# Kernel tuning notes

Hardware: AMD Instinct MI355X
Metric: run time of the kernel (lower is better)

The kernel has to match this reference:

```python
import jax, jax.numpy as jnp
import numpy as np

N = 200000      # total points
B = 4           # number of point clouds
C_IN = 128
C_OUT = 256
GRID = 0.05
EPS = 1e-5      # BatchNorm eps


def setup_inputs() -> dict:
    key = jax.random.key(0)
    ks = jax.random.split(key, 9)
    xyz = jax.random.uniform(ks[0], (1, N, 3), dtype=jnp.float32)
    features = jax.random.normal(ks[1], (1, N, C_IN), dtype=jnp.float32)
    offset = jnp.array([50000, 100000, 150000, 200000], dtype=jnp.int32)
    W1 = jax.random.normal(ks[2], (C_OUT, C_IN), dtype=jnp.float32) * 0.02
    b1 = jax.random.normal(ks[3], (C_OUT,), dtype=jnp.float32) * 0.01
    gamma = jax.random.uniform(ks[4], (C_OUT,), dtype=jnp.float32, minval=0.5, maxval=1.5)
    beta = jax.random.normal(ks[5], (C_OUT,), dtype=jnp.float32) * 0.1
    W2 = jax.random.normal(ks[6], (C_OUT, C_OUT), dtype=jnp.float32) * 0.02
    b2 = jax.random.normal(ks[7], (C_OUT,), dtype=jnp.float32) * 0.01
    return {"xyz": xyz, "features": features, "offset": offset,
            "W1": W1, "b1": b1, "gamma": gamma, "beta": beta, "W2": W2, "b2": b2}


def _offset2batch(offset, n):
    counts = jnp.diff(jnp.concatenate([jnp.zeros((1,), offset.dtype), offset]))
    return jnp.repeat(jnp.arange(offset.shape[0], dtype=jnp.int32), counts,
                      total_repeat_length=n)


def reference(xyz, features, offset, W1, b1, gamma, beta, W2, b2):
    pos = xyz[0]          # [N, 3]
    x = features[0]       # [N, C_IN]
    batch = _offset2batch(offset, pos.shape[0])  # [N]

    # fc: 1x1 conv == linear; BatchNorm1d in training mode (batch stats, biased var)
    h = x @ W1.T + b1                                   # [N, C_OUT]
    mu = h.mean(axis=0)
    var = h.var(axis=0)
    h = (h - mu) / jnp.sqrt(var + EPS) * gamma + beta
    h = jax.nn.relu(h)
    feats = h @ W2.T + b2                               # [N, C_OUT]

    # per-batch min corner (start)
    start = jax.ops.segment_min(pos, batch, num_segments=B)   # [B, 3]

    # voxel grid clustering
    coords = jnp.floor((pos - start[batch]) / GRID).astype(jnp.int32)  # [N, 3] >= 0
    dims = coords.max(axis=0) + 1
    lin = ((batch * dims[0] + coords[:, 0]) * dims[1] + coords[:, 1]) * dims[2] + coords[:, 2]

    uniq, inv, counts = jnp.unique(lin, return_inverse=True, return_counts=True)
    M = uniq.shape[0]

    # segment_csr mean / max over voxels (order-independent, equals sorted CSR reduce)
    xyz_out = jax.ops.segment_sum(pos, inv, num_segments=M) / counts[:, None].astype(pos.dtype)
    feat_out = jax.ops.segment_max(feats, inv, num_segments=M)

    seg_batch = jax.ops.segment_max(batch, inv, num_segments=M)
    offset_out = jnp.cumsum(jnp.bincount(seg_batch, length=B)).astype(offset.dtype)

    return (xyz_out[None], feat_out[None], offset_out, inv)
```

## Files before the change

### kernel.cpp

```cpp
#include <hip/hip_runtime.h>
#include <stdint.h>

#define GRID_SZ 0.05f
#define BN_EPS 1e-5f
#define FLAG_MAGIC 0x7FECA110

typedef __attribute__((ext_vector_type(8))) short bf16x8;
typedef __attribute__((ext_vector_type(4))) float f32x4;

#define WS_START   0
#define WS_DIMS    64
#define WS_CHSUM   128
#define WS_CHSQ    1152
#define WS_AC      2176
#define WS_BC      3200
#define WS_W1B     4224
#define WS_W2B     69760
#define WS_GRAM    200832
#define WS_CSUM    266368
#define WS_HIST    266880
#define WS_RANK    529024
#define WS_CURS    791296
#define WS_BSUM    1053440
#define WS_XYZS    1053952
#define WS_LIN     1840384
#define WS_PERM    2640384
#define WS_XB      3440384

__device__ __forceinline__ short f2bf(float f) {
  unsigned u = __float_as_uint(f);
  u += 0x7FFFu + ((u >> 16) & 1u);
  return (short)(u >> 16);
}

__device__ __forceinline__ bf16x8 load_frag(const float* p) {
  f32x4 a = *(const f32x4*)p;
  f32x4 b = *(const f32x4*)(p + 4);
  bf16x8 r;
  r[0] = f2bf(a[0]); r[1] = f2bf(a[1]); r[2] = f2bf(a[2]); r[3] = f2bf(a[3]);
  r[4] = f2bf(b[0]); r[5] = f2bf(b[1]); r[6] = f2bf(b[2]); r[7] = f2bf(b[3]);
  return r;
}

__device__ __forceinline__ int batch_of(int p, const int* offs, int nb) {
  int b = 0;
  while (b < nb - 1 && p >= offs[b]) b++;
  return b;
}

__device__ __forceinline__ float dec16(unsigned e) {
  unsigned us = (e & 0x8000u) ? (e & 0x7FFFu) : (~e & 0xFFFFu);
  return __uint_as_float(us << 16);
}

__global__ void k_conv(const float* __restrict__ src, short* __restrict__ dst, size_t n8) {
  size_t i = (size_t)blockIdx.x * blockDim.x + threadIdx.x;
  size_t stride = (size_t)gridDim.x * blockDim.x;
  for (; i < n8; i += stride)
    *(bf16x8*)(dst + i * 8) = load_frag(src + i * 8);
}

__global__ void k_convw(const float* __restrict__ W1, const float* __restrict__ W2,
                        short* __restrict__ W1b, short* __restrict__ W2b) {
  int i = blockIdx.x * blockDim.x + threadIdx.x;
  if (i < 4096) *(bf16x8*)(W1b + i * 8) = load_frag(W1 + i * 8);
  else { int j = i - 4096; *(bf16x8*)(W2b + j * 8) = load_frag(W2 + j * 8); }
}

__global__ void k_init(unsigned* featU, size_t featN, int* hist, float* xyzs,
                       float* chsum, float* chsq, float* gram, float* csum,
                       unsigned* gstart, int* gdims) {
  size_t i = (size_t)blockIdx.x * blockDim.x + threadIdx.x;
  size_t stride = (size_t)gridDim.x * blockDim.x;
  for (size_t j = i; j < featN; j += stride) featU[j] = 0u;
  for (size_t j = i; j < 65536; j += stride) hist[j] = 0;
  for (size_t j = i; j < 65536u * 3; j += stride) xyzs[j] = 0.f;
  for (size_t j = i; j < 16384; j += stride) gram[j] = 0.f;
  if (i < 256) { chsum[i] = 0.f; chsq[i] = 0.f; }
  if (i < 128) csum[i] = 0.f;
  if (i < 12) gstart[i] = 0x7F800000u;
  if (i < 3) gdims[i] = 0;
}

__global__ void k_min(const float* __restrict__ pos, const int* __restrict__ offs,
                      int N, int nb, unsigned* gstart) {
  __shared__ unsigned smin[12];
  int tid = threadIdx.x;
  if (tid < 12) smin[tid] = 0x7F800000u;
  __syncthreads();
  int p = blockIdx.x * blockDim.x + tid;
  if (p < N) {
    int b = batch_of(p, offs, nb);
    for (int c = 0; c < 3; c++)
      atomicMin(&smin[b * 3 + c], __float_as_uint(pos[p * 3 + c]));
  }
  __syncthreads();
  if (tid < 3 * nb) atomicMin(&gstart[tid], smin[tid]);
}

__global__ void k_dims(const float* __restrict__ pos, const int* __restrict__ offs,
                       int N, int nb, const unsigned* gstart, int* gdims) {
  __shared__ int sd[3];
  int tid = threadIdx.x;
  if (tid < 3) sd[tid] = 0;
  __syncthreads();
  int p = blockIdx.x * blockDim.x + tid;
  if (p < N) {
    int b = batch_of(p, offs, nb);
    for (int c = 0; c < 3; c++) {
      float s = __uint_as_float(gstart[b * 3 + c]);
      int cc = (int)floorf((pos[p * 3 + c] - s) / GRID_SZ);
      atomicMax(&sd[c], cc);
    }
  }
  __syncthreads();
  if (tid < 3) atomicMax(&gdims[tid], sd[tid]);
}

__global__ void k_hist(const float* __restrict__ pos, const int* __restrict__ offs,
                       int N, int nb, const unsigned* gstart, const int* gdims,
                       int* lin, int* hist, float* xyzs) {
  int p = blockIdx.x * blockDim.x + threadIdx.x;
  if (p >= N) return;
  int b = batch_of(p, offs, nb);
  int d0 = gdims[0] + 1, d1 = gdims[1] + 1, d2 = gdims[2] + 1;
  int c[3];
  for (int i = 0; i < 3; i++) {
    float s = __uint_as_float(gstart[b * 3 + i]);
    c[i] = (int)floorf((pos[p * 3 + i] - s) / GRID_SZ);
  }
  int li = ((b * d0 + c[0]) * d1 + c[1]) * d2 + c[2];
  if (li < 0 || li >= 65536) li = 0;
  lin[p] = li;
  atomicAdd(&hist[li], 1);
  atomicAdd(&xyzs[li * 3 + 0], pos[p * 3 + 0]);
  atomicAdd(&xyzs[li * 3 + 1], pos[p * 3 + 1]);
  atomicAdd(&xyzs[li * 3 + 2], pos[p * 3 + 2]);
}

__global__ __launch_bounds__(1024) void k_scanA(const int* __restrict__ hist,
                                                const int* __restrict__ gdims, int nb,
                                                int2* bsum) {
  __shared__ int so[16], sc2[16];
  int d0 = gdims[0] + 1, d1 = gdims[1] + 1, d2 = gdims[2] + 1;
  int bins = nb * d0 * d1 * d2;
  if (bins > 65536) bins = 65536;
  int i = blockIdx.x * 1024 + threadIdx.x;
  int o = 0, c = 0;
  if (i < bins) { int h = hist[i]; o = (h > 0); c = h; }
  for (int d = 1; d < 64; d <<= 1) { o += __shfl_xor(o, d); c += __shfl_xor(c, d); }
  int w = threadIdx.x >> 6;
  if ((threadIdx.x & 63) == 0) { so[w] = o; sc2[w] = c; }
  __syncthreads();
  if (threadIdx.x == 0) {
    int O = 0, C = 0;
    for (int k = 0; k < 16; k++) { O += so[k]; C += sc2[k]; }
    bsum[blockIdx.x] = make_int2(O, C);
  }
}

__global__ __launch_bounds__(1024) void k_scanB(const int* __restrict__ hist,
                                                const int* __restrict__ gdims, int nb,
                                                const int2* __restrict__ bsum,
                                                int* rank, int* cursor) {
  __shared__ int so[1024], sc2[1024];
  __shared__ int sbase[2];
  int d0 = gdims[0] + 1, d1 = gdims[1] + 1, d2 = gdims[2] + 1;
  int bins = nb * d0 * d1 * d2;
  if (bins > 65536) bins = 65536;
  int b = blockIdx.x;
  int tid = threadIdx.x;
  if (tid == 0) {
    int O = 0, C = 0;
    for (int k = 0; k < b; k++) { int2 s = bsum[k]; O += s.x; C += s.y; }
    sbase[0] = O; sbase[1] = C;
  }
  int i = b * 1024 + tid;
  int h = (i < bins) ? hist[i] : 0;
  int o = (h > 0), c = h;
  so[tid] = o; sc2[tid] = c;
  __syncthreads();
  for (int off = 1; off < 1024; off <<= 1) {
    int vo = (tid >= off) ? so[tid - off] : 0;
    int vc = (tid >= off) ? sc2[tid - off] : 0;
    __syncthreads();
    so[tid] += vo; sc2[tid] += vc;
    __syncthreads();
  }
  if (i < bins) {
    rank[i]   = sbase[0] + so[tid] - o;
    cursor[i] = sbase[1] + sc2[tid] - c;
  }
  if (i == bins - 1) rank[bins] = sbase[0] + so[tid];
}

__global__ void k_scatter(const int* __restrict__ lin, const int* __restrict__ rank,
                          int* cursor, int N, int* __restrict__ perm,
                          float* __restrict__ out_inv) {
  int p = blockIdx.x * blockDim.x + threadIdx.x;
  if (p >= N) return;
  int li = lin[p];
  out_inv[p] = (float)rank[li];
  int slot = atomicAdd(&cursor[li], 1);
  perm[slot] = p;
}

__global__ void k_voxfin(const int* __restrict__ hist, const int* __restrict__ rank,
                         const float* __restrict__ xyzs, const int* __restrict__ gdims,
                         int nb, float* out_xyz, float* out_off) {
  int d0 = gdims[0] + 1, d1 = gdims[1] + 1, d2 = gdims[2] + 1;
  int dxyz = d0 * d1 * d2;
  int bins = nb * dxyz;
  if (bins > 65536) bins = 65536;
  int i = blockIdx.x * blockDim.x + threadIdx.x;
  if (blockIdx.x == 0 && (int)threadIdx.x < nb) {
    int t = (int)threadIdx.x;
    int idx = (t + 1) * dxyz; if (idx > bins) idx = bins;
    out_off[t] = (float)rank[idx];
  }
  if (i >= bins) return;
  int cnt = hist[i];
  if (cnt <= 0) return;
  int v = rank[i];
  float fc = (float)cnt;
  out_xyz[v * 3 + 0] = xyzs[i * 3 + 0] / fc;
  out_xyz[v * 3 + 1] = xyzs[i * 3 + 1] / fc;
  out_xyz[v * 3 + 2] = xyzs[i * 3 + 2] / fc;
}

#define GCHUNK 1024
__global__ __launch_bounds__(256, 2) void k_gram(const short* __restrict__ Xb, int N,
                                                 float* __restrict__ gram,
                                                 float* __restrict__ csum) {
  __shared__ short xt[128 * 72];
  __shared__ float lcs[128];
  int tid = threadIdx.x;
  int wid = tid >> 6, lane = tid & 63;
  int lr = lane & 15, lg = lane >> 4;
  int base = blockIdx.x * GCHUNK;
  int cg = tid & 7;
  float cs[16];
#pragma unroll
  for (int j = 0; j < 16; j++) cs[j] = 0.f;
  f32x4 acc[2][8];
#pragma unroll
  for (int a = 0; a < 2; a++)
#pragma unroll
    for (int b = 0; b < 8; b++) acc[a][b] = (f32x4){0.f, 0.f, 0.f, 0.f};

  for (int k0 = 0; k0 < GCHUNK; k0 += 64) {
    __syncthreads();
#pragma unroll
    for (int it = 0; it < 2; it++) {
      int task = tid + it * 256;
      int r = task >> 3;
      int row = base + k0 + r;
      bf16x8 v0 = {0,0,0,0,0,0,0,0}, v1 = {0,0,0,0,0,0,0,0};
      if (row < N) {
        const short* src = Xb + (size_t)row * 128 + cg * 16;
        v0 = *(const bf16x8*)src;
        v1 = *(const bf16x8*)(src + 8);
      }
#pragma unroll
      for (int j = 0; j < 8; j++) {
        cs[j]     += __uint_as_float(((unsigned)(unsigned short)v0[j]) << 16);
        cs[j + 8] += __uint_as_float(((unsigned)(unsigned short)v1[j]) << 16);
      }
      int rs = r ^ (cg << 3);
#pragma unroll
      for (int j = 0; j < 8; j++) {
        xt[(cg * 16 + j) * 72 + rs]     = v0[j];
        xt[(cg * 16 + 8 + j) * 72 + rs] = v1[j];
      }
    }
    __syncthreads();
#pragma unroll
    for (int ks = 0; ks < 2; ks++) {
      int kk = ks * 32 + lg * 8;
      bf16x8 f[8], af[2];
#pragma unroll
      for (int s = 0; s < 8; s++)
        f[s] = *(const bf16x8*)(xt + (s * 16 + lr) * 72 + (kk ^ (s << 3)));
#pragma unroll
      for (int a = 0; a < 2; a++) {
        int ti = wid * 2 + a;
        af[a] = *(const bf16x8*)(xt + (ti * 16 + lr) * 72 + (kk ^ (ti << 3)));
      }
#pragma unroll
      for (int a = 0; a < 2; a++)
#pragma unroll
        for (int b = 0; b < 8; b++)
          acc[a][b] = __builtin_amdgcn_mfma_f32_16x16x32_bf16(af[a], f[b], acc[a][b], 0, 0, 0);
    }
  }
#pragma unroll
  for (int a = 0; a < 2; a++)
#pragma unroll
    for (int b = 0; b < 8; b++)
#pragma unroll
      for (int r_ = 0; r_ < 4; r_++) {
        int ci = (wid * 2 + a) * 16 + lg * 4 + r_;
        int cj = b * 16 + lr;
        atomicAdd(&gram[ci * 128 + cj], acc[a][b][r_]);
      }
  if (tid < 128) lcs[tid] = 0.f;
  __syncthreads();
#pragma unroll
  for (int j = 0; j < 16; j++) atomicAdd(&lcs[cg * 16 + j], cs[j]);
  __syncthreads();
  if (tid < 128) atomicAdd(&csum[tid], lcs[tid]);
}

__global__ __launch_bounds__(128) void k_finalizeG(const float* __restrict__ gram,
                                                   const float* __restrict__ csum,
                                                   const float* __restrict__ W1,
                                                   const float* __restrict__ b1,
                                                   const float* __restrict__ gamma,
                                                   const float* __restrict__ beta,
                                                   int N, float* Ac, float* Bc) {
  __shared__ float w[128], red[128], red2[128];
  int c = blockIdx.x, j = threadIdx.x;
  w[j] = W1[c * 128 + j];
  __syncthreads();
  float t = 0.f;
  for (int k = 0; k < 128; k++) t += gram[k * 128 + j] * w[k];
  red[j]  = t * w[j];
  red2[j] = w[j] * csum[j];
  __syncthreads();
  for (int off = 64; off > 0; off >>= 1) {
    if (j < off) { red[j] += red[j + off]; red2[j] += red2[j + off]; }
    __syncthreads();
  }
  if (j == 0) {
    float fn = (float)N;
    float q  = red[0] / fn;
    float md = red2[0] / fn;
    float b  = b1[c];
    float mu = md + b;
    float e2 = q + 2.f * b * md + b * b;
    float var = e2 - mu * mu;
    float s = gamma[c] * rsqrtf(var + BN_EPS);
    Ac[c] = s;
    Bc[c] = (b - mu) * s + beta[c];
  }
}

__global__ __launch_bounds__(256) void k_statsA(const float* __restrict__ X,
                                                const short* __restrict__ W1b,
                                                const float* __restrict__ b1, int N,
                                                float* chsum, float* chsq) {
  int tid = threadIdx.x;
  int wid = tid >> 6, lane = tid & 63;
  int lr = lane & 15, lg = lane >> 4;
  int p0 = blockIdx.x * 64;
  int wcol = wid * 64;
  f32x4 acc[4][4] = {};
  for (int kk = 0; kk < 4; kk++) {
    int k = kk * 32 + lg * 8;
    bf16x8 af[4], bfr[4];
    for (int m = 0; m < 4; m++) {
      int row = p0 + m * 16 + lr; if (row >= N) row = N - 1;
      af[m] = load_frag(X + (size_t)row * 128 + k);
    }
    for (int n = 0; n < 4; n++)
      bfr[n] = *(const bf16x8*)(W1b + (size_t)(wcol + n * 16 + lr) * 128 + k);
    for (int m = 0; m < 4; m++)
      for (int n = 0; n < 4; n++)
        acc[m][n] = __builtin_amdgcn_mfma_f32_16x16x32_bf16(af[m], bfr[n], acc[m][n], 0, 0, 0);
  }
  for (int n = 0; n < 4; n++) {
    int c = wcol + n * 16 + lr;
    float bv = b1[c];
    float s1 = 0.f, s2 = 0.f;
    for (int m = 0; m < 4; m++)
      for (int r = 0; r < 4; r++) {
        int row = p0 + m * 16 + lg * 4 + r;
        if (row < N) {
          float h = acc[m][n][r] + bv;
          s1 += h; s2 += h * h;
        }
      }
    s1 += __shfl_xor(s1, 16); s2 += __shfl_xor(s2, 16);
    s1 += __shfl_xor(s1, 32); s2 += __shfl_xor(s2, 32);
    if (lg == 0) { atomicAdd(&chsum[c], s1); atomicAdd(&chsq[c], s2); }
  }
}

__global__ void k_finalize(const float* chsum, const float* chsq, const float* b1,
                           const float* gamma, const float* beta, int N,
                           float* Ac, float* Bc) {
  int c = threadIdx.x;
  float fn = (float)N;
  float mu = chsum[c] / fn;
  float var = chsq[c] / fn - mu * mu;
  float s = gamma[c] * rsqrtf(var + BN_EPS);
  Ac[c] = s;
  Bc[c] = (b1[c] - mu) * s + beta[c];
}

template <bool XBF>
__global__ __launch_bounds__(256, 3) void k_gemmB(const float* __restrict__ X,
                                                  const short* __restrict__ Xb,
                                                  const short* __restrict__ W1b,
                                                  const short* __restrict__ W2b,
                                                  const float* __restrict__ b2,
                                                  const float* __restrict__ Ac,
                                                  const float* __restrict__ Bc,
                                                  const int* __restrict__ perm,
                                                  const int* __restrict__ lin,
                                                  const int* __restrict__ rank,
                                                  int N, unsigned* __restrict__ featU,
                                                  int* __restrict__ bflag) {
  __shared__ char smem[64 * 264 * 2];
  __shared__ int vox_s[64];
  __shared__ int perm_s[64];
  char* axt  = smem;
  char* ylds = smem;
  unsigned short* lmax = (unsigned short*)smem;

  int tid = threadIdx.x;
  int wid = tid >> 6, lane = tid & 63;
  int lr = lane & 15, lg = lane >> 4;
  int p0 = blockIdx.x * 64;
  int wcol = wid * 64;

  if (tid < 64) {
    int s = p0 + tid;
    int pp = perm[(s < N) ? s : (N - 1)];
    perm_s[tid] = pp;
    vox_s[tid] = (s < N) ? rank[lin[pp]] : -1;
  }
  __syncthreads();

  {
    int row = tid >> 2, chunk = tid & 3;
    int prow = perm_s[row];
    int base = row * 256 + chunk * 64;
    int sw = (row & 7) << 4;
    bf16x8 a0, a1, a2, a3;
    if (XBF) {
      const short* src = Xb + (size_t)prow * 128 + chunk * 32;
      a0 = *(const bf16x8*)(src);
      a1 = *(const bf16x8*)(src + 8);
      a2 = *(const bf16x8*)(src + 16);
      a3 = *(const bf16x8*)(src + 24);
    } else {
      const float* src = X + (size_t)prow * 128 + chunk * 32;
      a0 = load_frag(src);
      a1 = load_frag(src + 8);
      a2 = load_frag(src + 16);
      a3 = load_frag(src + 24);
    }
    *(bf16x8*)(axt + ((base)      ^ sw)) = a0;
    *(bf16x8*)(axt + ((base + 16) ^ sw)) = a1;
    *(bf16x8*)(axt + ((base + 32) ^ sw)) = a2;
    *(bf16x8*)(axt + ((base + 48) ^ sw)) = a3;
  }
  __syncthreads();

  f32x4 acc[4][4] = {};
  for (int kk = 0; kk < 4; kk++) {
    int kbyte = kk * 64 + lg * 16;
    bf16x8 af[4], bfr[4];
    int sw = (lr & 7) << 4;
    for (int m = 0; m < 4; m++) {
      int rowA = m * 16 + lr;
      af[m] = *(const bf16x8*)(axt + ((rowA * 256 + kbyte) ^ sw));
    }
    int k = kk * 32 + lg * 8;
    for (int n = 0; n < 4; n++)
      bfr[n] = *(const bf16x8*)(W1b + (size_t)(wcol + n * 16 + lr) * 128 + k);
    for (int m = 0; m < 4; m++)
      for (int n = 0; n < 4; n++)
        acc[m][n] = __builtin_amdgcn_mfma_f32_16x16x32_bf16(af[m], bfr[n], acc[m][n], 0, 0, 0);
  }
  __syncthreads();

  for (int n = 0; n < 4; n++) {
    int c = wcol + n * 16 + lr;
    float Av = Ac[c], Bv = Bc[c];
    int colb = c * 2;
    for (int m = 0; m < 4; m++)
      for (int r = 0; r < 4; r++) {
        int row = m * 16 + lg * 4 + r;
        float y = fmaxf(acc[m][n][r] * Av + Bv, 0.0f);
        int addr = (row * 512 + colb) ^ ((row & 7) << 4);
        *(short*)(ylds + addr) = f2bf(y);
      }
  }
  __syncthreads();

  f32x4 acc2[4][4] = {};
  for (int kk = 0; kk < 8; kk++) {
    int k = kk * 32 + lg * 8;
    int kb = k * 2;
    bf16x8 af[4], bfr[4];
    for (int m = 0; m < 4; m++) {
      int row = m * 16 + lr;
      af[m] = *(const bf16x8*)(ylds + ((row * 512 + kb) ^ ((row & 7) << 4)));
    }
    for (int n = 0; n < 4; n++)
      bfr[n] = *(const bf16x8*)(W2b + (size_t)(wcol + n * 16 + lr) * 256 + k);
    for (int m = 0; m < 4; m++)
      for (int n = 0; n < 4; n++)
        acc2[m][n] = __builtin_amdgcn_mfma_f32_16x16x32_bf16(af[m], bfr[n], acc2[m][n], 0, 0, 0);
  }
  __syncthreads();

  for (int n = 0; n < 4; n++) {
    int c = wcol + n * 16 + lr;
    float bv = b2[c];
    for (int m = 0; m < 4; m++)
      for (int r = 0; r < 4; r++) {
        int row = m * 16 + lg * 4 + r;
        unsigned us = (unsigned)(unsigned short)f2bf(acc2[m][n][r] + bv);
        us = (us & 0x8000u) ? (~us & 0xFFFFu) : (us | 0x8000u);
        lmax[row * 264 + c] = (unsigned short)us;
      }
  }
  __syncthreads();

  int nrows = N - p0; if (nrows > 64) nrows = 64;
  int c = tid;
  unsigned run = 0;
  int vprev = vox_s[0];
  int run_start = 0;
  for (int row = 0; row < nrows; row++) {
    int v = vox_s[row];
    if (v != vprev) {
      size_t idx = (size_t)vprev * 256 + c;
      if (run_start > 0) {
        ((float*)featU)[idx] = dec16(run);
      } else {
        atomicMax(&featU[idx], run << 16);
        if (tid == 0) bflag[vprev] = FLAG_MAGIC;
      }
      run = 0; vprev = v; run_start = row;
    }
    run = max(run, (unsigned)lmax[row * 264 + c]);
  }
  atomicMax(&featU[(size_t)vprev * 256 + c], run << 16);
  if (tid == 0) bflag[vprev] = FLAG_MAGIC;
}

__global__ void k_decode(unsigned* featU, const int* __restrict__ bflag, size_t n) {
  size_t i = (size_t)blockIdx.x * blockDim.x + threadIdx.x;
  size_t stride = (size_t)gridDim.x * blockDim.x;
  for (; i < n; i += stride) {
    if (bflag[i >> 8] == FLAG_MAGIC) {
      unsigned e = featU[i] >> 16;
      ((float*)featU)[i] = dec16(e);
    }
  }
}

extern "C" void kernel_launch(void* const* d_in, const int* in_sizes, int n_in,
                              void* d_out, int out_size, void* d_ws, size_t ws_size,
                              hipStream_t stream) {
  const float* xyz   = (const float*)d_in[0];
  const float* X     = (const float*)d_in[1];
  const int*   offs  = (const int*)d_in[2];
  const float* W1    = (const float*)d_in[3];
  const float* b1    = (const float*)d_in[4];
  const float* gamma = (const float*)d_in[5];
  const float* beta  = (const float*)d_in[6];
  const float* W2    = (const float*)d_in[7];
  const float* b2    = (const float*)d_in[8];

  int N  = in_sizes[0] / 3;
  int nb = in_sizes[2];
  int M  = (out_size - nb - N) / 259;
  if (M <= 0) return;

  char* ws = (char*)d_ws;
  unsigned* gstart = (unsigned*)(ws + WS_START);
  int*   gdims  = (int*)(ws + WS_DIMS);
  float* chsum  = (float*)(ws + WS_CHSUM);
  float* chsq   = (float*)(ws + WS_CHSQ);
  float* Ac     = (float*)(ws + WS_AC);
  float* Bc     = (float*)(ws + WS_BC);
  short* W1b    = (short*)(ws + WS_W1B);
  short* W2b    = (short*)(ws + WS_W2B);
  float* gram   = (float*)(ws + WS_GRAM);
  float* csum   = (float*)(ws + WS_CSUM);
  int*   hist   = (int*)(ws + WS_HIST);
  int*   rank   = (int*)(ws + WS_RANK);
  int*   cursor = (int*)(ws + WS_CURS);
  int2*  bsum   = (int2*)(ws + WS_BSUM);
  float* xyzs   = (float*)(ws + WS_XYZS);
  int*   lin    = (int*)(ws + WS_LIN);
  int*   perm   = (int*)(ws + WS_PERM);
  short* Xb     = (short*)(ws + WS_XB);

  size_t req = (size_t)WS_XB + (size_t)N * 128 * 2;
  bool xbf = ws_size >= req;

  float* out_xyz  = (float*)d_out;
  float* out_feat = out_xyz + (size_t)3 * M;
  float* out_off  = out_feat + (size_t)M * 256;
  float* out_inv  = out_off + nb;
  unsigned* featU = (unsigned*)out_feat;

  int npb = (N + 255) / 256;
  int ngb = (N + 63) / 64;
  int ngr = (N + GCHUNK - 1) / GCHUNK;

  hipLaunchKernelGGL(k_init, dim3(2048), dim3(256), 0, stream,
                     featU, (size_t)M * 256, hist, xyzs, chsum, chsq, gram, csum,
                     gstart, gdims);
  hipLaunchKernelGGL(k_convw, dim3(24), dim3(256), 0, stream, W1, W2, W1b, W2b);
  if (xbf) {
    hipLaunchKernelGGL(k_conv, dim3(4096), dim3(256), 0, stream, X, Xb, (size_t)N * 128 / 8);
    hipLaunchKernelGGL(k_gram, dim3(ngr), dim3(256), 0, stream, Xb, N, gram, csum);
  }
  hipLaunchKernelGGL(k_min, dim3(npb), dim3(256), 0, stream, xyz, offs, N, nb, gstart);
  hipLaunchKernelGGL(k_dims, dim3(npb), dim3(256), 0, stream, xyz, offs, N, nb, gstart, gdims);
  hipLaunchKernelGGL(k_hist, dim3(npb), dim3(256), 0, stream,
                     xyz, offs, N, nb, gstart, gdims, lin, hist, xyzs);
  hipLaunchKernelGGL(k_scanA, dim3(64), dim3(1024), 0, stream, hist, gdims, nb, bsum);
  hipLaunchKernelGGL(k_scanB, dim3(64), dim3(1024), 0, stream,
                     hist, gdims, nb, bsum, rank, cursor);
  hipLaunchKernelGGL(k_voxfin, dim3(256), dim3(256), 0, stream,
                     hist, rank, xyzs, gdims, nb, out_xyz, out_off);
  hipLaunchKernelGGL(k_scatter, dim3(npb), dim3(256), 0, stream,
                     lin, rank, cursor, N, perm, out_inv);
  if (xbf) {
    hipLaunchKernelGGL(k_finalizeG, dim3(256), dim3(128), 0, stream,
                       gram, csum, W1, b1, gamma, beta, N, Ac, Bc);
    hipLaunchKernelGGL((k_gemmB<true>), dim3(ngb), dim3(256), 0, stream,
                       X, Xb, W1b, W2b, b2, Ac, Bc, perm, lin, rank, N, featU, cursor);
  } else {
    hipLaunchKernelGGL(k_statsA, dim3(ngb), dim3(256), 0, stream,
                       X, W1b, b1, N, chsum, chsq);
    hipLaunchKernelGGL(k_finalize, dim3(1), dim3(256), 0, stream,
                       chsum, chsq, b1, gamma, beta, N, Ac, Bc);
    hipLaunchKernelGGL((k_gemmB<false>), dim3(ngb), dim3(256), 0, stream,
                       X, Xb, W1b, W2b, b2, Ac, Bc, perm, lin, rank, N, featU, cursor);
  }
  hipLaunchKernelGGL(k_decode, dim3(2048), dim3(256), 0, stream,
                     featU, cursor, (size_t)M * 256);
}
```

Measured before the change: 298.6 us.

## Fuse bf16 conversion into voxel scatter and merge small preprocessing kernels

The fp32-to-bf16 conversion of the input features moves into the scatter kernel, which now writes each point's row directly into voxel-sorted order. The GEMM can then read contiguous rows and the precomputed voxel id instead of gathering through a permutation. The weight conversion is folded into the init kernel, and the grid dimensions are derived from per-batch max coordinates gathered alongside the min in one pass, which removes the separate dims kernel. Each scatter thread now writes 256 bytes to a scattered destination row, which may coalesce poorly. The Gram statistics kernel now runs after the scatter, so it can no longer overlap the earlier stages.

```diff
diff --git a/kernel.cpp b/kernel.cpp
--- a/kernel.cpp
+++ b/kernel.cpp
@@ -9,7 +9,7 @@
 typedef __attribute__((ext_vector_type(4))) float f32x4;
 
 #define WS_START   0
-#define WS_DIMS    64
+#define WS_DIMS    96
 #define WS_CHSUM   128
 #define WS_CHSQ    1152
 #define WS_AC      2176
@@ -53,25 +53,31 @@
   return __uint_as_float(us << 16);
 }
 
-__global__ void k_conv(const float* __restrict__ src, short* __restrict__ dst, size_t n8) {
+__device__ __forceinline__ void dims_of(const unsigned* gstart, int nb,
+                                        int& m0, int& m1, int& m2) {
+  m0 = 0; m1 = 0; m2 = 0;
+  for (int b = 0; b < nb; b++) {
+    float s0 = __uint_as_float(gstart[b * 3 + 0]);
+    float s1 = __uint_as_float(gstart[b * 3 + 1]);
+    float s2 = __uint_as_float(gstart[b * 3 + 2]);
+    float x0 = __uint_as_float(gstart[12 + b * 3 + 0]);
+    float x1 = __uint_as_float(gstart[12 + b * 3 + 1]);
+    float x2 = __uint_as_float(gstart[12 + b * 3 + 2]);
+    m0 = max(m0, (int)floorf((x0 - s0) / GRID_SZ));
+    m1 = max(m1, (int)floorf((x1 - s1) / GRID_SZ));
+    m2 = max(m2, (int)floorf((x2 - s2) / GRID_SZ));
+  }
+}
+
+__global__ void k_init(unsigned* featU, size_t featN, int* hist, float* xyzs,
+                       float* chsum, float* chsq, float* gram, float* csum,
+                       unsigned* gstart,
+                       const float* __restrict__ W1, const float* __restrict__ W2,
+                       short* __restrict__ W1b, short* __restrict__ W2b) {
   size_t i = (size_t)blockIdx.x * blockDim.x + threadIdx.x;
   size_t stride = (size_t)gridDim.x * blockDim.x;
-  for (; i < n8; i += stride)
-    *(bf16x8*)(dst + i * 8) = load_frag(src + i * 8);
-}
-
-__global__ void k_convw(const float* __restrict__ W1, const float* __restrict__ W2,
-                        short* __restrict__ W1b, short* __restrict__ W2b) {
-  int i = blockIdx.x * blockDim.x + threadIdx.x;
   if (i < 4096) *(bf16x8*)(W1b + i * 8) = load_frag(W1 + i * 8);
-  else { int j = i - 4096; *(bf16x8*)(W2b + j * 8) = load_frag(W2 + j * 8); }
-}
-
-__global__ void k_init(unsigned* featU, size_t featN, int* hist, float* xyzs,
-                       float* chsum, float* chsq, float* gram, float* csum,
-                       unsigned* gstart, int* gdims) {
-  size_t i = (size_t)blockIdx.x * blockDim.x + threadIdx.x;
-  size_t stride = (size_t)gridDim.x * blockDim.x;
+  else if (i < 12288) { size_t j = i - 4096; *(bf16x8*)(W2b + j * 8) = load_frag(W2 + j * 8); }
   for (size_t j = i; j < featN; j += stride) featU[j] = 0u;
   for (size_t j = i; j < 65536; j += stride) hist[j] = 0;
   for (size_t j = i; j < 65536u * 3; j += stride) xyzs[j] = 0.f;
@@ -79,51 +85,41 @@
   if (i < 256) { chsum[i] = 0.f; chsq[i] = 0.f; }
   if (i < 128) csum[i] = 0.f;
   if (i < 12) gstart[i] = 0x7F800000u;
-  if (i < 3) gdims[i] = 0;
+  else if (i < 24) gstart[i] = 0u;
 }
 
 __global__ void k_min(const float* __restrict__ pos, const int* __restrict__ offs,
                       int N, int nb, unsigned* gstart) {
-  __shared__ unsigned smin[12];
+  __shared__ unsigned smin[12], smax[12];
   int tid = threadIdx.x;
-  if (tid < 12) smin[tid] = 0x7F800000u;
-  __syncthreads();
-  int p = blockIdx.x * blockDim.x + tid;
-  if (p < N) {
-    int b = batch_of(p, offs, nb);
-    for (int c = 0; c < 3; c++)
-      atomicMin(&smin[b * 3 + c], __float_as_uint(pos[p * 3 + c]));
-  }
-  __syncthreads();
-  if (tid < 3 * nb) atomicMin(&gstart[tid], smin[tid]);
-}
-
-__global__ void k_dims(const float* __restrict__ pos, const int* __restrict__ offs,
-                       int N, int nb, const unsigned* gstart, int* gdims) {
-  __shared__ int sd[3];
-  int tid = threadIdx.x;
-  if (tid < 3) sd[tid] = 0;
+  if (tid < 12) { smin[tid] = 0x7F800000u; smax[tid] = 0u; }
   __syncthreads();
   int p = blockIdx.x * blockDim.x + tid;
   if (p < N) {
     int b = batch_of(p, offs, nb);
     for (int c = 0; c < 3; c++) {
-      float s = __uint_as_float(gstart[b * 3 + c]);
-      int cc = (int)floorf((pos[p * 3 + c] - s) / GRID_SZ);
-      atomicMax(&sd[c], cc);
-    }
-  }
-  __syncthreads();
-  if (tid < 3) atomicMax(&gdims[tid], sd[tid]);
+      unsigned u = __float_as_uint(pos[p * 3 + c]);
+      atomicMin(&smin[b * 3 + c], u);
+      atomicMax(&smax[b * 3 + c], u);
+    }
+  }
+  __syncthreads();
+  if (tid < 3 * nb) {
+    atomicMin(&gstart[tid], smin[tid]);
+    atomicMax(&gstart[12 + tid], smax[tid]);
+  }
 }
 
 __global__ void k_hist(const float* __restrict__ pos, const int* __restrict__ offs,
-                       int N, int nb, const unsigned* gstart, const int* gdims,
-                       int* lin, int* hist, float* xyzs) {
+                       int N, int nb, const unsigned* gstart,
+                       int* lin, int* hist, float* xyzs, int* gdims) {
+  int m0, m1, m2;
+  dims_of(gstart, nb, m0, m1, m2);
   int p = blockIdx.x * blockDim.x + threadIdx.x;
+  if (blockIdx.x == 0 && threadIdx.x == 0) { gdims[0] = m0; gdims[1] = m1; gdims[2] = m2; }
   if (p >= N) return;
   int b = batch_of(p, offs, nb);
-  int d0 = gdims[0] + 1, d1 = gdims[1] + 1, d2 = gdims[2] + 1;
+  int d0 = m0 + 1, d1 = m1 + 1, d2 = m2 + 1;
   int c[3];
   for (int i = 0; i < 3; i++) {
     float s = __uint_as_float(gstart[b * 3 + i]);
@@ -194,15 +190,27 @@
   if (i == bins - 1) rank[bins] = sbase[0] + so[tid];
 }
 
+template <bool XBF>
 __global__ void k_scatter(const int* __restrict__ lin, const int* __restrict__ rank,
-                          int* cursor, int N, int* __restrict__ perm,
+                          int* cursor, int N, const float* __restrict__ X,
+                          short* __restrict__ Xb, int* __restrict__ permvox,
                           float* __restrict__ out_inv) {
   int p = blockIdx.x * blockDim.x + threadIdx.x;
   if (p >= N) return;
   int li = lin[p];
-  out_inv[p] = (float)rank[li];
+  int r = rank[li];
+  out_inv[p] = (float)r;
   int slot = atomicAdd(&cursor[li], 1);
-  perm[slot] = p;
+  if (XBF) {
+    permvox[slot] = r;
+    const float* src = X + (size_t)p * 128;
+    short* dst = Xb + (size_t)slot * 128;
+#pragma unroll
+    for (int j = 0; j < 16; j++)
+      *(bf16x8*)(dst + j * 8) = load_frag(src + j * 8);
+  } else {
+    permvox[slot] = p;
+  }
 }
 
 __global__ void k_voxfin(const int* __restrict__ hist, const int* __restrict__ rank,
@@ -406,7 +414,7 @@
                                                   const float* __restrict__ b2,
                                                   const float* __restrict__ Ac,
                                                   const float* __restrict__ Bc,
-                                                  const int* __restrict__ perm,
+                                                  const int* __restrict__ permvox,
                                                   const int* __restrict__ lin,
                                                   const int* __restrict__ rank,
                                                   int N, unsigned* __restrict__ featU,
@@ -426,25 +434,30 @@
 
   if (tid < 64) {
     int s = p0 + tid;
-    int pp = perm[(s < N) ? s : (N - 1)];
-    perm_s[tid] = pp;
-    vox_s[tid] = (s < N) ? rank[lin[pp]] : -1;
+    if (XBF) {
+      vox_s[tid] = (s < N) ? permvox[s] : -1;
+    } else {
+      int pp = permvox[(s < N) ? s : (N - 1)];
+      perm_s[tid] = pp;
+      vox_s[tid] = (s < N) ? rank[lin[pp]] : -1;
+    }
   }
   __syncthreads();
 
   {
     int row = tid >> 2, chunk = tid & 3;
-    int prow = perm_s[row];
     int base = row * 256 + chunk * 64;
     int sw = (row & 7) << 4;
     bf16x8 a0, a1, a2, a3;
     if (XBF) {
-      const short* src = Xb + (size_t)prow * 128 + chunk * 32;
+      int grow = p0 + row; if (grow >= N) grow = N - 1;
+      const short* src = Xb + (size_t)grow * 128 + chunk * 32;
       a0 = *(const bf16x8*)(src);
       a1 = *(const bf16x8*)(src + 8);
       a2 = *(const bf16x8*)(src + 16);
       a3 = *(const bf16x8*)(src + 24);
     } else {
+      int prow = perm_s[row];
       const float* src = X + (size_t)prow * 128 + chunk * 32;
       a0 = load_frag(src);
       a1 = load_frag(src + 8);
@@ -589,7 +602,7 @@
   int2*  bsum   = (int2*)(ws + WS_BSUM);
   float* xyzs   = (float*)(ws + WS_XYZS);
   int*   lin    = (int*)(ws + WS_LIN);
-  int*   perm   = (int*)(ws + WS_PERM);
+  int*   permvox = (int*)(ws + WS_PERM);
   short* Xb     = (short*)(ws + WS_XB);
 
   size_t req = (size_t)WS_XB + (size_t)N * 128 * 2;
@@ -607,35 +620,32 @@
 
   hipLaunchKernelGGL(k_init, dim3(2048), dim3(256), 0, stream,
                      featU, (size_t)M * 256, hist, xyzs, chsum, chsq, gram, csum,
-                     gstart, gdims);
-  hipLaunchKernelGGL(k_convw, dim3(24), dim3(256), 0, stream, W1, W2, W1b, W2b);
-  if (xbf) {
-    hipLaunchKernelGGL(k_conv, dim3(4096), dim3(256), 0, stream, X, Xb, (size_t)N * 128 / 8);
-    hipLaunchKernelGGL(k_gram, dim3(ngr), dim3(256), 0, stream, Xb, N, gram, csum);
-  }
+                     gstart, W1, W2, W1b, W2b);
   hipLaunchKernelGGL(k_min, dim3(npb), dim3(256), 0, stream, xyz, offs, N, nb, gstart);
-  hipLaunchKernelGGL(k_dims, dim3(npb), dim3(256), 0, stream, xyz, offs, N, nb, gstart, gdims);
   hipLaunchKernelGGL(k_hist, dim3(npb), dim3(256), 0, stream,
-                     xyz, offs, N, nb, gstart, gdims, lin, hist, xyzs);
+                     xyz, offs, N, nb, gstart, lin, hist, xyzs, gdims);
   hipLaunchKernelGGL(k_scanA, dim3(64), dim3(1024), 0, stream, hist, gdims, nb, bsum);
   hipLaunchKernelGGL(k_scanB, dim3(64), dim3(1024), 0, stream,
                      hist, gdims, nb, bsum, rank, cursor);
   hipLaunchKernelGGL(k_voxfin, dim3(256), dim3(256), 0, stream,
                      hist, rank, xyzs, gdims, nb, out_xyz, out_off);
-  hipLaunchKernelGGL(k_scatter, dim3(npb), dim3(256), 0, stream,
-                     lin, rank, cursor, N, perm, out_inv);
   if (xbf) {
+    hipLaunchKernelGGL((k_scatter<true>), dim3(npb), dim3(256), 0, stream,
+                       lin, rank, cursor, N, X, Xb, permvox, out_inv);
+    hipLaunchKernelGGL(k_gram, dim3(ngr), dim3(256), 0, stream, Xb, N, gram, csum);
     hipLaunchKernelGGL(k_finalizeG, dim3(256), dim3(128), 0, stream,
                        gram, csum, W1, b1, gamma, beta, N, Ac, Bc);
     hipLaunchKernelGGL((k_gemmB<true>), dim3(ngb), dim3(256), 0, stream,
-                       X, Xb, W1b, W2b, b2, Ac, Bc, perm, lin, rank, N, featU, cursor);
+                       X, Xb, W1b, W2b, b2, Ac, Bc, permvox, lin, rank, N, featU, cursor);
   } else {
+    hipLaunchKernelGGL((k_scatter<false>), dim3(npb), dim3(256), 0, stream,
+                       lin, rank, cursor, N, X, Xb, permvox, out_inv);
     hipLaunchKernelGGL(k_statsA, dim3(ngb), dim3(256), 0, stream,
                        X, W1b, b1, N, chsum, chsq);
     hipLaunchKernelGGL(k_finalize, dim3(1), dim3(256), 0, stream,
                        chsum, chsq, b1, gamma, beta, N, Ac, Bc);
     hipLaunchKernelGGL((k_gemmB<false>), dim3(ngb), dim3(256), 0, stream,
-                       X, Xb, W1b, W2b, b2, Ac, Bc, perm, lin, rank, N, featU, cursor);
+                       X, Xb, W1b, W2b, b2, Ac, Bc, permvox, lin, rank, N, featU, cursor);
   }
   hipLaunchKernelGGL(k_decode, dim3(2048), dim3(256), 0, stream,
                      featU, cursor, (size_t)M * 256);
```

New measurement: 298.3 us. No clear change (-0.1%).
